# Optimization experiments

Measured on AMD Instinct MI355X. Metric: run time of the kernel, lower is better.

Reference implementation:

```python
import jax, jax.numpy as jnp
import numpy as np

N = 4096      # nodes
F = 512       # input_dim
D = 512       # output_dim
H = 8         # n_heads
d = D // H    # per-head out_sz


def setup_inputs() -> dict:
    key = jax.random.key(0)
    ks = jax.random.split(key, 6)
    x = jax.random.normal(ks[0], (N, F), dtype=jnp.float32)
    adj = (jax.random.uniform(ks[1], (N, N)) < 0.01).astype(jnp.float32)
    adj = jnp.maximum(adj, jnp.eye(N, dtype=jnp.float32))
    # per-head params: weight transform W, attention vectors a1/a2 (conv1d k=1 -> dot) with biases
    W = jax.random.normal(ks[2], (H, F, d), dtype=jnp.float32) * 0.05
    a1 = jax.random.normal(ks[3], (H, d), dtype=jnp.float32) * 0.05
    a2 = jax.random.normal(ks[4], (H, d), dtype=jnp.float32) * 0.05
    b1 = jnp.zeros((H,), dtype=jnp.float32)
    b2 = jnp.zeros((H,), dtype=jnp.float32)
    return {"x": x, "adj": adj, "W": W, "a1": a1, "b1": b1, "a2": a2, "b2": b2}


def reference(x, adj, W, a1, b1, a2, b2):
    # per-node linear transform for all heads: [H, N, d]
    seq_fts = jnp.einsum('nf,hfd->hnd', x, W)
    # attention logits components (conv1d(out=1,k=1) == dot + bias): [H, N]
    f1 = jnp.einsum('hnd,hd->hn', seq_fts, a1) + b1[:, None]
    f2 = jnp.einsum('hnd,hd->hn', seq_fts, a2) + b2[:, None]
    # logits = adj * f1_i + adj * f2_j  (adj acts multiplicatively AND as sparsity mask)
    logits = adj[None, :, :] * f1[:, :, None] + adj[None, :, :] * f2[:, None, :]
    lrelu = jnp.maximum(0.2 * logits, logits)  # leaky_relu alpha=0.2
    # sparse softmax over adjacency nonzeros (tf.sparse_softmax over from_dense pattern)
    mask = adj != 0
    scores = jnp.where(mask[None, :, :], lrelu, -jnp.inf)
    coefs = jax.nn.softmax(scores, axis=-1)           # [H, N, N], zero off-mask
    vals = jnp.einsum('hnm,hmd->hnd', coefs, seq_fts)  # sparse-dense matmul per head
    # concat heads on feature axis, batch dim of 1, elu activation
    h = jnp.transpose(vals, (1, 0, 2)).reshape(N, H * d)[None, :, :]
    return jax.nn.elu(h)
```

## Files before the change

### kernel.cpp

```cpp
#include <hip/hip_runtime.h>
#include <math.h>

#define N_NODES 4096
#define F_DIM   512
#define D_DIM   512
#define H_HEADS 8
#define HD      64
#define CAP     160

typedef __attribute__((ext_vector_type(8))) short short8;
typedef __attribute__((ext_vector_type(4))) float f32x4;

__device__ __forceinline__ unsigned short f2bf(float f) {
    unsigned int u = __builtin_bit_cast(unsigned int, f);
    return (unsigned short)((u + 0x7FFFu + ((u >> 16) & 1u)) >> 16);
}
__device__ __forceinline__ float bflo(unsigned int u) {
    return __builtin_bit_cast(float, u << 16);
}
__device__ __forceinline__ float bfhi(unsigned int u) {
    return __builtin_bit_cast(float, u & 0xffff0000u);
}

__global__ __launch_bounds__(256) void conv_inputs(const float* __restrict__ x,
                                                   const float* __restrict__ W,
                                                   unsigned short* __restrict__ xb,
                                                   unsigned short* __restrict__ Bt) {
    if (blockIdx.x < 1024) {
        const int t = blockIdx.x * 256 + threadIdx.x;
        const float4 v0 = *(const float4*)&x[t * 8];
        const float4 v1 = *(const float4*)&x[t * 8 + 4];
        unsigned short o[8] = {f2bf(v0.x), f2bf(v0.y), f2bf(v0.z), f2bf(v0.w),
                               f2bf(v1.x), f2bf(v1.y), f2bf(v1.z), f2bf(v1.w)};
        *(uint4*)&xb[t * 8] = *(const uint4*)o;
    } else {
        const int t = (blockIdx.x - 1024) * 256 + threadIdx.x;
        const int n = t >> 6;
        const int kb = (t & 63) * 8;
        const int h = n >> 6, dd = n & 63;
        const float* src = W + (size_t)h * F_DIM * HD + dd;
        unsigned short o[8];
        #pragma unroll
        for (int q = 0; q < 8; ++q) o[q] = f2bf(src[(size_t)(kb + q) * HD]);
        *(uint4*)&Bt[(size_t)n * F_DIM + kb] = *(const uint4*)o;
    }
}

__global__ __launch_bounds__(256) void gemm_mfma(const unsigned short* __restrict__ A,
                                                 const unsigned short* __restrict__ Bt,
                                                 const float* __restrict__ a1,
                                                 const float* __restrict__ b1,
                                                 const float* __restrict__ a2,
                                                 const float* __restrict__ b2,
                                                 unsigned short* __restrict__ seqb,
                                                 float* __restrict__ f1t,
                                                 float* __restrict__ f2t) {
    __shared__ unsigned short As[64][40];
    __shared__ unsigned short Bs[64][40];
    __shared__ float sF[2][64][2];

    const int tid  = threadIdx.x;
    const int lane = tid & 63;
    const int w    = tid >> 6;
    const int wr   = w >> 1, wc = w & 1;
    const int i0   = blockIdx.x * 64;
    const int h    = blockIdx.y;
    const int n0   = h * 64;

    const int ar = tid >> 2;
    const int ac = (tid & 3) * 8;

    const int rlane = lane & 15;
    const int q     = lane >> 4;
    const int klane = q * 8;

    f32x4 acc[2][2] = {};

    for (int k0 = 0; k0 < F_DIM; k0 += 32) {
        const uint4 av = *(const uint4*)&A[(size_t)(i0 + ar) * F_DIM + k0 + ac];
        const uint4 bv = *(const uint4*)&Bt[(size_t)(n0 + ar) * F_DIM + k0 + ac];
        __syncthreads();
        *(uint4*)&As[ar][ac] = av;
        *(uint4*)&Bs[ar][ac] = bv;
        __syncthreads();

        short8 a_frag[2], b_frag[2];
        #pragma unroll
        for (int mi = 0; mi < 2; ++mi)
            a_frag[mi] = *(const short8*)&As[wr * 32 + mi * 16 + rlane][klane];
        #pragma unroll
        for (int ni = 0; ni < 2; ++ni)
            b_frag[ni] = *(const short8*)&Bs[wc * 32 + ni * 16 + rlane][klane];
        #pragma unroll
        for (int mi = 0; mi < 2; ++mi)
            #pragma unroll
            for (int ni = 0; ni < 2; ++ni)
                acc[mi][ni] = __builtin_amdgcn_mfma_f32_16x16x32_bf16(
                    a_frag[mi], b_frag[ni], acc[mi][ni], 0, 0, 0);
    }

    #pragma unroll
    for (int mi = 0; mi < 2; ++mi)
        #pragma unroll
        for (int ni = 0; ni < 2; ++ni)
            #pragma unroll
            for (int r = 0; r < 4; ++r) {
                const int row = i0 + wr * 32 + mi * 16 + q * 4 + r;
                const int col = n0 + wc * 32 + ni * 16 + rlane;
                seqb[(size_t)row * D_DIM + col] = f2bf(acc[mi][ni][r]);
            }

    float a1v[2], a2v[2];
    #pragma unroll
    for (int ni = 0; ni < 2; ++ni) {
        const int c = wc * 32 + ni * 16 + rlane;
        a1v[ni] = a1[h * HD + c];
        a2v[ni] = a2[h * HD + c];
    }
    #pragma unroll
    for (int mi = 0; mi < 2; ++mi)
        #pragma unroll
        for (int r = 0; r < 4; ++r) {
            float s1 = acc[mi][0][r] * a1v[0] + acc[mi][1][r] * a1v[1];
            float s2 = acc[mi][0][r] * a2v[0] + acc[mi][1][r] * a2v[1];
            #pragma unroll
            for (int m = 1; m < 16; m <<= 1) {
                s1 += __shfl_xor(s1, m, 64);
                s2 += __shfl_xor(s2, m, 64);
            }
            if (rlane == 0) {
                const int rl = wr * 32 + mi * 16 + q * 4 + r;
                sF[0][rl][wc] = s1;
                sF[1][rl][wc] = s2;
            }
        }
    __syncthreads();
    if (tid < 64) {
        const int row = i0 + tid;
        f1t[row * 8 + h] = sF[0][tid][0] + sF[0][tid][1] + b1[h];
        f2t[row * 8 + h] = sF[1][tid][0] + sF[1][tid][1] + b2[h];
    }
}

__global__ __launch_bounds__(128) void attn(const float* __restrict__ adj,
                                            const unsigned short* __restrict__ seqb,
                                            const float* __restrict__ f1t,
                                            const float* __restrict__ f2t,
                                            float* __restrict__ out) {
    __shared__ int   sIdx[CAP];
    __shared__ float sP[CAP][8];
    __shared__ float sRed[2][8];
    __shared__ float sAcc[64][8];
    __shared__ int   sTot[2];

    const int i    = blockIdx.x;
    const int tid  = threadIdx.x;
    const int lane = tid & 63;
    const int w    = tid >> 6;
    const float* arow = adj + (size_t)i * N_NODES;

    const int c0 = tid * 32;
    f32x4 vq[8];
    #pragma unroll
    for (int q = 0; q < 8; ++q)
        vq[q] = *(const f32x4*)&arow[c0 + q * 4];
    float vv[32];
    #pragma unroll
    for (int q = 0; q < 8; ++q) {
        vv[q * 4 + 0] = vq[q].x; vv[q * 4 + 1] = vq[q].y;
        vv[q * 4 + 2] = vq[q].z; vv[q * 4 + 3] = vq[q].w;
    }
    int n_t = 0;
    #pragma unroll
    for (int q = 0; q < 32; ++q) n_t += (vv[q] != 0.0f) ? 1 : 0;

    int incl = n_t;
    #pragma unroll
    for (int off = 1; off < 64; off <<= 1) {
        int u = __shfl_up(incl, off, 64);
        if (lane >= off) incl += u;
    }
    if (lane == 63) sTot[w] = incl;
    __syncthreads();
    const int w0tot = sTot[0];
    const int cnt   = w0tot + sTot[1];
    int pos = (w ? w0tot : 0) + incl - n_t;
    if (cnt <= CAP) {
        #pragma unroll
        for (int q = 0; q < 32; ++q) {
            if (vv[q] != 0.0f) { sIdx[pos] = c0 + q; ++pos; }
        }
    }
    __syncthreads();

    const float4 f1a = *(const float4*)&f1t[i * 8];
    const float4 f1b = *(const float4*)&f1t[i * 8 + 4];
    const float f1r[8] = {f1a.x, f1a.y, f1a.z, f1a.w, f1b.x, f1b.y, f1b.z, f1b.w};

    const int h8 = lane >> 3;
    float acc[8] = {0.f, 0.f, 0.f, 0.f, 0.f, 0.f, 0.f, 0.f};
    float myinv;

    if (cnt <= CAP) {
        float m[8];
        #pragma unroll
        for (int h = 0; h < 8; ++h) m[h] = -INFINITY;
        for (int jj = tid; jj < cnt; jj += 128) {
            const int j = sIdx[jj];
            const float4 fa = *(const float4*)&f2t[j * 8];
            const float4 fb = *(const float4*)&f2t[j * 8 + 4];
            const float f2r[8] = {fa.x, fa.y, fa.z, fa.w, fb.x, fb.y, fb.z, fb.w};
            float L[8];
            #pragma unroll
            for (int h = 0; h < 8; ++h) {
                float v = f1r[h] + f2r[h];
                v = fmaxf(v, 0.2f * v);
                L[h] = v;
                m[h] = fmaxf(m[h], v);
            }
            f32x4 La = {L[0], L[1], L[2], L[3]};
            f32x4 Lb = {L[4], L[5], L[6], L[7]};
            *(f32x4*)&sP[jj][0] = La;
            *(f32x4*)&sP[jj][4] = Lb;
        }
        #pragma unroll
        for (int off = 32; off; off >>= 1)
            #pragma unroll
            for (int h = 0; h < 8; ++h)
                m[h] = fmaxf(m[h], __shfl_xor(m[h], off, 64));
        if (lane == 0) {
            f32x4 ma = {m[0], m[1], m[2], m[3]};
            f32x4 mb = {m[4], m[5], m[6], m[7]};
            *(f32x4*)&sRed[w][0] = ma;
            *(f32x4*)&sRed[w][4] = mb;
        }
        __syncthreads();
        #pragma unroll
        for (int h = 0; h < 8; ++h) m[h] = fmaxf(sRed[0][h], sRed[1][h]);
        __syncthreads();

        float s[8] = {0.f, 0.f, 0.f, 0.f, 0.f, 0.f, 0.f, 0.f};
        for (int jj = tid; jj < cnt; jj += 128) {
            const f32x4 La = *(const f32x4*)&sP[jj][0];
            const f32x4 Lb = *(const f32x4*)&sP[jj][4];
            const float L[8] = {La.x, La.y, La.z, La.w, Lb.x, Lb.y, Lb.z, Lb.w};
            float e[8];
            #pragma unroll
            for (int h = 0; h < 8; ++h) {
                e[h] = __expf(L[h] - m[h]);
                s[h] += e[h];
            }
            f32x4 ea = {e[0], e[1], e[2], e[3]};
            f32x4 eb = {e[4], e[5], e[6], e[7]};
            *(f32x4*)&sP[jj][0] = ea;
            *(f32x4*)&sP[jj][4] = eb;
        }
        #pragma unroll
        for (int off = 32; off; off >>= 1)
            #pragma unroll
            for (int h = 0; h < 8; ++h)
                s[h] += __shfl_xor(s[h], off, 64);
        if (lane == 0) {
            f32x4 sa = {s[0], s[1], s[2], s[3]};
            f32x4 sb = {s[4], s[5], s[6], s[7]};
            *(f32x4*)&sRed[w][0] = sa;
            *(f32x4*)&sRed[w][4] = sb;
        }
        __syncthreads();
        myinv = 1.0f / (sRed[0][h8] + sRed[1][h8]);

        const int cnt2 = (cnt + 1) >> 1;
        const int jlo = w ? cnt2 : 0;
        const int jhi = w ? cnt  : cnt2;
        const char* __restrict__ vbase = (const char*)seqb + lane * 16;
        int jj = jlo;
        for (; jj + 4 <= jhi; jj += 4) {
            const int4 j4 = *(const int4*)&sIdx[jj];
            const float p0 = sP[jj + 0][h8];
            const float p1 = sP[jj + 1][h8];
            const float p2 = sP[jj + 2][h8];
            const float p3 = sP[jj + 3][h8];
            const uint4 u0 = *(const uint4*)(vbase + ((size_t)j4.x << 10));
            const uint4 u1 = *(const uint4*)(vbase + ((size_t)j4.y << 10));
            const uint4 u2 = *(const uint4*)(vbase + ((size_t)j4.z << 10));
            const uint4 u3 = *(const uint4*)(vbase + ((size_t)j4.w << 10));
            const unsigned int w0[4] = {u0.x, u0.y, u0.z, u0.w};
            const unsigned int w1[4] = {u1.x, u1.y, u1.z, u1.w};
            const unsigned int w2[4] = {u2.x, u2.y, u2.z, u2.w};
            const unsigned int w3[4] = {u3.x, u3.y, u3.z, u3.w};
            #pragma unroll
            for (int k = 0; k < 4; ++k) {
                acc[k * 2 + 0] = fmaf(p0, bflo(w0[k]), acc[k * 2 + 0]);
                acc[k * 2 + 1] = fmaf(p0, bfhi(w0[k]), acc[k * 2 + 1]);
                acc[k * 2 + 0] = fmaf(p1, bflo(w1[k]), acc[k * 2 + 0]);
                acc[k * 2 + 1] = fmaf(p1, bfhi(w1[k]), acc[k * 2 + 1]);
                acc[k * 2 + 0] = fmaf(p2, bflo(w2[k]), acc[k * 2 + 0]);
                acc[k * 2 + 1] = fmaf(p2, bfhi(w2[k]), acc[k * 2 + 1]);
                acc[k * 2 + 0] = fmaf(p3, bflo(w3[k]), acc[k * 2 + 0]);
                acc[k * 2 + 1] = fmaf(p3, bfhi(w3[k]), acc[k * 2 + 1]);
            }
        }
        for (; jj < jhi; ++jj) {
            const int j = sIdx[jj];
            const float p = sP[jj][h8];
            const uint4 u = *(const uint4*)(vbase + ((size_t)j << 10));
            const unsigned int wv[4] = {u.x, u.y, u.z, u.w};
            #pragma unroll
            for (int k = 0; k < 4; ++k) {
                acc[k * 2 + 0] = fmaf(p, bflo(wv[k]), acc[k * 2 + 0]);
                acc[k * 2 + 1] = fmaf(p, bfhi(wv[k]), acc[k * 2 + 1]);
            }
        }
    } else {
        float m[8];
        #pragma unroll
        for (int h = 0; h < 8; ++h) m[h] = -INFINITY;
        for (int j = tid; j < N_NODES; j += 128) {
            if (arow[j] != 0.0f) {
                const float4 fa = *(const float4*)&f2t[j * 8];
                const float4 fb = *(const float4*)&f2t[j * 8 + 4];
                const float f2r[8] = {fa.x, fa.y, fa.z, fa.w, fb.x, fb.y, fb.z, fb.w};
                #pragma unroll
                for (int h = 0; h < 8; ++h) {
                    float v = f1r[h] + f2r[h];
                    v = fmaxf(v, 0.2f * v);
                    m[h] = fmaxf(m[h], v);
                }
            }
        }
        #pragma unroll
        for (int off = 32; off; off >>= 1)
            #pragma unroll
            for (int h = 0; h < 8; ++h)
                m[h] = fmaxf(m[h], __shfl_xor(m[h], off, 64));
        if (lane == 0) {
            f32x4 ma = {m[0], m[1], m[2], m[3]};
            f32x4 mb = {m[4], m[5], m[6], m[7]};
            *(f32x4*)&sRed[w][0] = ma;
            *(f32x4*)&sRed[w][4] = mb;
        }
        __syncthreads();
        #pragma unroll
        for (int h = 0; h < 8; ++h) m[h] = fmaxf(sRed[0][h], sRed[1][h]);
        __syncthreads();

        float s[8] = {0.f, 0.f, 0.f, 0.f, 0.f, 0.f, 0.f, 0.f};
        for (int j = tid; j < N_NODES; j += 128) {
            if (arow[j] != 0.0f) {
                const float4 fa = *(const float4*)&f2t[j * 8];
                const float4 fb = *(const float4*)&f2t[j * 8 + 4];
                const float f2r[8] = {fa.x, fa.y, fa.z, fa.w, fb.x, fb.y, fb.z, fb.w};
                #pragma unroll
                for (int h = 0; h < 8; ++h) {
                    float v = f1r[h] + f2r[h];
                    v = fmaxf(v, 0.2f * v);
                    s[h] += __expf(v - m[h]);
                }
            }
        }
        #pragma unroll
        for (int off = 32; off; off >>= 1)
            #pragma unroll
            for (int h = 0; h < 8; ++h)
                s[h] += __shfl_xor(s[h], off, 64);
        if (lane == 0) {
            f32x4 sa = {s[0], s[1], s[2], s[3]};
            f32x4 sb = {s[4], s[5], s[6], s[7]};
            *(f32x4*)&sRed[w][0] = sa;
            *(f32x4*)&sRed[w][4] = sb;
        }
        __syncthreads();
        myinv = 1.0f / (sRed[0][h8] + sRed[1][h8]);
        const float mh = m[h8], f1h = f1r[h8];

        const char* __restrict__ vbase = (const char*)seqb + lane * 16;
        const int jlo = w * (N_NODES / 2), jhi = jlo + N_NODES / 2;
        for (int j = jlo; j < jhi; ++j) {
            if (arow[j] != 0.0f) {
                float v = f1h + f2t[j * 8 + h8];
                v = fmaxf(v, 0.2f * v);
                const float p = __expf(v - mh);
                const uint4 u = *(const uint4*)(vbase + ((size_t)j << 10));
                const unsigned int wv[4] = {u.x, u.y, u.z, u.w};
                #pragma unroll
                for (int k = 0; k < 4; ++k) {
                    acc[k * 2 + 0] = fmaf(p, bflo(wv[k]), acc[k * 2 + 0]);
                    acc[k * 2 + 1] = fmaf(p, bfhi(wv[k]), acc[k * 2 + 1]);
                }
            }
        }
    }

    if (w == 1) {
        f32x4 pa = {acc[0], acc[1], acc[2], acc[3]};
        f32x4 pb = {acc[4], acc[5], acc[6], acc[7]};
        *(f32x4*)&sAcc[lane][0] = pa;
        *(f32x4*)&sAcc[lane][4] = pb;
    }
    __syncthreads();
    if (w == 0) {
        float o[8];
        #pragma unroll
        for (int k = 0; k < 8; ++k) {
            const float v = (acc[k] + sAcc[lane][k]) * myinv;
            o[k] = (v > 0.f) ? v : expm1f(v);
        }
        f32x4 oa = {o[0], o[1], o[2], o[3]};
        f32x4 ob = {o[4], o[5], o[6], o[7]};
        float* dst = &out[(size_t)i * D_DIM + lane * 8];
        __builtin_nontemporal_store(oa, (f32x4*)dst);
        __builtin_nontemporal_store(ob, (f32x4*)(dst + 4));
    }
}

extern "C" void kernel_launch(void* const* d_in, const int* in_sizes, int n_in,
                              void* d_out, int out_size, void* d_ws, size_t ws_size,
                              hipStream_t stream) {
    const float* x   = (const float*)d_in[0];
    const float* adj = (const float*)d_in[1];
    const float* W   = (const float*)d_in[2];
    const float* a1  = (const float*)d_in[3];
    const float* b1  = (const float*)d_in[4];
    const float* a2  = (const float*)d_in[5];
    const float* b2  = (const float*)d_in[6];
    float* out = (float*)d_out;

    char* ws = (char*)d_ws;
    unsigned short* seqb = (unsigned short*)ws;
    unsigned short* xb   = (unsigned short*)(ws + (size_t)N_NODES * D_DIM * 2);
    unsigned short* Bt   = (unsigned short*)(ws + (size_t)N_NODES * D_DIM * 4);
    float* f1t = (float*)(ws + (size_t)N_NODES * D_DIM * 4 + (size_t)D_DIM * F_DIM * 2);
    float* f2t = f1t + (size_t)N_NODES * H_HEADS;

    conv_inputs<<<1152, 256, 0, stream>>>(x, W, xb, Bt);

    dim3 gg(N_NODES / 64, D_DIM / 64);
    gemm_mfma<<<gg, 256, 0, stream>>>(xb, Bt, a1, b1, a2, b2, seqb, f1t, f2t);

    attn<<<N_NODES, 128, 0, stream>>>(adj, seqb, f1t, f2t, out);
}
```

Baseline: 48.96 us.

## Move adjacency compaction into prep kernel ahead of GEMM

The scan of the dense adjacency row and the building of its nonzero index list move out of the attention kernel into the first prep kernel, which writes per-row index lists and counts to workspace. The attention kernel then only loads a short index list instead of streaming a 16KB row, and no longer needs a block-wide scan and barrier before starting. The aim is to put the 64MB adjacency read in a kernel that sits off the attention critical path and overlaps with the bf16 conversions. The cost is extra workspace traffic and a heavier prep launch.

```diff
diff --git a/kernel.cpp b/kernel.cpp
--- a/kernel.cpp
+++ b/kernel.cpp
@@ -22,19 +22,60 @@
     return __builtin_bit_cast(float, u & 0xffff0000u);
 }
 
-__global__ __launch_bounds__(256) void conv_inputs(const float* __restrict__ x,
-                                                   const float* __restrict__ W,
-                                                   unsigned short* __restrict__ xb,
-                                                   unsigned short* __restrict__ Bt) {
-    if (blockIdx.x < 1024) {
-        const int t = blockIdx.x * 256 + threadIdx.x;
+__global__ __launch_bounds__(256) void prep(const float* __restrict__ adj,
+                                            const float* __restrict__ x,
+                                            const float* __restrict__ W,
+                                            unsigned short* __restrict__ xb,
+                                            unsigned short* __restrict__ Bt,
+                                            int* __restrict__ rowIdx,
+                                            int* __restrict__ cntArr) {
+    const int b = blockIdx.x;
+    if (b < 1024) {
+        const int lane = threadIdx.x & 63;
+        const int w    = threadIdx.x >> 6;
+        const int r    = b * 4 + w;
+        const float* arow = adj + (size_t)r * N_NODES;
+
+        f32x4 vq[16];
+        #pragma unroll
+        for (int q = 0; q < 16; ++q)
+            vq[q] = *(const f32x4*)&arow[q * 256 + lane * 4];
+
+        unsigned long long mask = 0ull;
+        #pragma unroll
+        for (int q = 0; q < 16; ++q) {
+            if (vq[q].x != 0.0f) mask |= 1ull << (q * 4 + 0);
+            if (vq[q].y != 0.0f) mask |= 1ull << (q * 4 + 1);
+            if (vq[q].z != 0.0f) mask |= 1ull << (q * 4 + 2);
+            if (vq[q].w != 0.0f) mask |= 1ull << (q * 4 + 3);
+        }
+        const int n_t = __popcll(mask);
+        int incl = n_t;
+        #pragma unroll
+        for (int off = 1; off < 64; off <<= 1) {
+            int u = __shfl_up(incl, off, 64);
+            if (lane >= off) incl += u;
+        }
+        const int tot = __shfl(incl, 63, 64);
+        int pos = incl - n_t;
+        const int rbase = r * CAP;
+        while (mask) {
+            const int bit = __builtin_ctzll(mask);
+            mask &= mask - 1;
+            const int col = ((bit >> 2) << 8) + (lane << 2) + (bit & 3);
+            if (pos < CAP) rowIdx[rbase + pos] = col;
+            ++pos;
+        }
+        if (lane == 0) cntArr[r] = tot;
+    } else if (b < 2048) {
+        const int t = (b - 1024) * 256 + threadIdx.x;
         const float4 v0 = *(const float4*)&x[t * 8];
         const float4 v1 = *(const float4*)&x[t * 8 + 4];
         unsigned short o[8] = {f2bf(v0.x), f2bf(v0.y), f2bf(v0.z), f2bf(v0.w),
                                f2bf(v1.x), f2bf(v1.y), f2bf(v1.z), f2bf(v1.w)};
         *(uint4*)&xb[t * 8] = *(const uint4*)o;
     } else {
-        const int t = (blockIdx.x - 1024) * 256 + threadIdx.x;
+        const int t = (b - 2048) * 256 + threadIdx.x;
         const int n = t >> 6;
         const int kb = (t & 63) * 8;
         const int h = n >> 6, dd = n & 63;
@@ -146,50 +187,23 @@
                                             const unsigned short* __restrict__ seqb,
                                             const float* __restrict__ f1t,
                                             const float* __restrict__ f2t,
+                                            const int* __restrict__ rowIdx,
+                                            const int* __restrict__ cntArr,
                                             float* __restrict__ out) {
     __shared__ int   sIdx[CAP];
     __shared__ float sP[CAP][8];
     __shared__ float sRed[2][8];
     __shared__ float sAcc[64][8];
-    __shared__ int   sTot[2];
 
     const int i    = blockIdx.x;
     const int tid  = threadIdx.x;
     const int lane = tid & 63;
     const int w    = tid >> 6;
-    const float* arow = adj + (size_t)i * N_NODES;
-
-    const int c0 = tid * 32;
-    f32x4 vq[8];
-    #pragma unroll
-    for (int q = 0; q < 8; ++q)
-        vq[q] = *(const f32x4*)&arow[c0 + q * 4];
-    float vv[32];
-    #pragma unroll
-    for (int q = 0; q < 8; ++q) {
-        vv[q * 4 + 0] = vq[q].x; vv[q * 4 + 1] = vq[q].y;
-        vv[q * 4 + 2] = vq[q].z; vv[q * 4 + 3] = vq[q].w;
-    }
-    int n_t = 0;
-    #pragma unroll
-    for (int q = 0; q < 32; ++q) n_t += (vv[q] != 0.0f) ? 1 : 0;
-
-    int incl = n_t;
-    #pragma unroll
-    for (int off = 1; off < 64; off <<= 1) {
-        int u = __shfl_up(incl, off, 64);
-        if (lane >= off) incl += u;
-    }
-    if (lane == 63) sTot[w] = incl;
-    __syncthreads();
-    const int w0tot = sTot[0];
-    const int cnt   = w0tot + sTot[1];
-    int pos = (w ? w0tot : 0) + incl - n_t;
+
+    const int cnt = cntArr[i];
     if (cnt <= CAP) {
-        #pragma unroll
-        for (int q = 0; q < 32; ++q) {
-            if (vv[q] != 0.0f) { sIdx[pos] = c0 + q; ++pos; }
-        }
+        for (int jj = tid; jj < cnt; jj += 128)
+            sIdx[jj] = rowIdx[i * CAP + jj];
     }
     __syncthreads();
 
@@ -312,6 +326,7 @@
             }
         }
     } else {
+        const float* arow = adj + (size_t)i * N_NODES;
         float m[8];
         #pragma unroll
         for (int h = 0; h < 8; ++h) m[h] = -INFINITY;
@@ -431,11 +446,13 @@
     unsigned short* Bt   = (unsigned short*)(ws + (size_t)N_NODES * D_DIM * 4);
     float* f1t = (float*)(ws + (size_t)N_NODES * D_DIM * 4 + (size_t)D_DIM * F_DIM * 2);
     float* f2t = f1t + (size_t)N_NODES * H_HEADS;
-
-    conv_inputs<<<1152, 256, 0, stream>>>(x, W, xb, Bt);
+    int* rowIdx = (int*)(f2t + (size_t)N_NODES * H_HEADS);
+    int* cntArr = rowIdx + (size_t)N_NODES * CAP;
+
+    prep<<<2176, 256, 0, stream>>>(adj, x, W, xb, Bt, rowIdx, cntArr);
 
     dim3 gg(N_NODES / 64, D_DIM / 64);
     gemm_mfma<<<gg, 256, 0, stream>>>(xb, Bt, a1, b1, a2, b2, seqb, f1t, f2t);
 
-    attn<<<N_NODES, 128, 0, stream>>>(adj, seqb, f1t, f2t, out);
-}
+    attn<<<N_NODES, 128, 0, stream>>>(adj, seqb, f1t, f2t, rowIdx, cntArr, out);
+}
```

Measured after the change: 48.15 us. No clear change (-1.7%).
